# Optimization experiments

Hardware: AMD Instinct MI355X
Metric: run time of the kernel (lower is better)

The kernel has to match this reference:

```python
import jax, jax.numpy as jnp
import numpy as np

BATCH, INPUTDIM, OUTDIM, GRIDSIZE = 4096, 256, 256, 64


def setup_inputs() -> dict:
    key = jax.random.key(0)
    k1, k2 = jax.random.split(key)
    x = jax.random.normal(k1, (BATCH, INPUTDIM), dtype=jnp.float32)
    # xavier_uniform over (2, outdim, inputdim, gridsize): fan_in = inputdim*gridsize, fan_out = outdim*gridsize
    fan_in = INPUTDIM * GRIDSIZE
    fan_out = OUTDIM * GRIDSIZE
    limit = float(np.sqrt(6.0 / (fan_in + fan_out)))
    fouriercoeffs = jax.random.uniform(
        k2, (2, OUTDIM, INPUTDIM, GRIDSIZE), dtype=jnp.float32,
        minval=-limit, maxval=limit)
    bias = jnp.zeros((1, OUTDIM), dtype=jnp.float32)
    return {"x": x, "fouriercoeffs": fouriercoeffs, "bias": bias}


def reference(x, fouriercoeffs, bias):
    # x: [B, inputdim]; fouriercoeffs: [2, outdim, inputdim, gridsize]; bias: [1, outdim]
    # gridsize_param is clamp/round'ed to an int in torch -> static = initial_gridsize here.
    G = fouriercoeffs.shape[-1]
    k = jnp.arange(1, G + 1, dtype=x.dtype)        # [G] frequencies 1..G
    xk = x[:, :, None] * k                          # [B, inputdim, G]
    c = jnp.cos(xk)                                 # [B, inputdim, G]
    s = jnp.sin(xk)                                 # [B, inputdim, G]
    # Fused contraction over (inputdim, gridsize) -- avoids the naive
    # [B, outdim, inputdim, gridsize] broadcast tensor of the torch code.
    y = (jnp.einsum('big,oig->bo', c, fouriercoeffs[0])
         + jnp.einsum('big,oig->bo', s, fouriercoeffs[1])
         + bias)                                    # [B, outdim]
    return y
```

## Files before the change

### kernel.cpp

```cpp
#include <hip/hip_runtime.h>
#include <hip/hip_bf16.h>


typedef __attribute__((ext_vector_type(8))) short short8;
typedef __attribute__((ext_vector_type(16))) float f32x16;

#define SPLITK 16
#define ICHUNK (256 / SPLITK)

#define INV2PI 0.15915494309189535f

__device__ __forceinline__ unsigned short f2bf(float f) {
    unsigned u = __builtin_bit_cast(unsigned, f);
    u += 0x7fffu + ((u >> 16) & 1u);
    return (unsigned short)(u >> 16);
}
#if __has_builtin(__builtin_amdgcn_cvt_pk_bf16_f32)
typedef __attribute__((ext_vector_type(2))) __bf16 bf16x2_t;
__device__ __forceinline__ unsigned pkbf16(float a, float b) {
    bf16x2_t v = __builtin_amdgcn_cvt_pk_bf16_f32(a, b);
    return __builtin_bit_cast(unsigned, v);
}
#else
__device__ __forceinline__ unsigned pkbf16(float a, float b) {
    unsigned ua = __builtin_bit_cast(unsigned, a) + 0x8000u;
    unsigned ub = __builtin_bit_cast(unsigned, b) + 0x8000u;
    return __builtin_amdgcn_perm(ub, ua, 0x07060302u);
}
#endif

__device__ __forceinline__ void dbl2(float c, float s, float& co, float& so) {
    float t = c + c;
    co = __builtin_fmaf(t, c, -1.f);
    so = t * s;
}
__device__ __forceinline__ void rot2(float c, float s, float cr, float sr,
                                     float& co, float& so) {
    float t = s * sr;
    co = __builtin_fmaf(c, cr, -t);
    float u = s * cr;
    so = __builtin_fmaf(c, sr, u);
}

__device__ __forceinline__ short8 chain8(float m1, float fm1, float f0) {
    unsigned r[4];
    float vp = fm1, v = f0;
    #pragma unroll
    for (int h = 0; h < 4; ++h) {
        float v1 = __builtin_fmaf(m1, v, -vp);
        r[h] = pkbf16(v, v1);
        float v2 = __builtin_fmaf(m1, v1, -v);
        vp = v1; v = v2;
    }
    uint4 u; u.x = r[0]; u.y = r[1]; u.z = r[2]; u.w = r[3];
    return __builtin_bit_cast(short8, u);
}

__device__ __forceinline__ void async_load16(const void* g, void* l) {
    __builtin_amdgcn_global_load_lds(
        (const __attribute__((address_space(1))) unsigned int*)g,
        (__attribute__((address_space(3))) unsigned int*)l,
        16, 0, 0);
}

__global__ __launch_bounds__(512) void prep_kernel(
    const float* __restrict__ fc, unsigned short* __restrict__ ws2)
{
    __shared__ unsigned pk[512][36];
    const int i = blockIdx.x;
    const int t = threadIdx.x;
    const int rr  = t >> 4;
    const int l16 = t & 15;

    #pragma unroll
    for (int p = 0; p < 16; ++p) {
        int r = p * 32 + rr;
        const float4* src =
            (const float4*)(fc + ((size_t)r * 256 + i) * 64) + l16;
        float4 v = *src;
        pk[r][l16 * 2]     = pkbf16(v.x, v.y);
        pk[r][l16 * 2 + 1] = pkbf16(v.z, v.w);
    }
    __syncthreads();

    #pragma unroll
    for (int gg = 0; gg < 8; ++gg) {
        int gi = gg * 512 + t;
        int sog = gi >> 6, ll = gi & 63;
        int ks = sog >> 3, cb = sog & 7;
        int o  = cb * 32 + (ll & 31);
        int kb = ks * 16 + (ll >> 5) * 8;
        int tt = kb >> 6, g0 = kb & 63;
        int r = tt * 256 + o;
        int c = g0 >> 1;
        uint4 v;
        v.x = pk[r][c]; v.y = pk[r][c + 1];
        v.z = pk[r][c + 2]; v.w = pk[r][c + 3];
        ((uint4*)ws2)[(size_t)i * 4096 + gi] = v;
    }
}

__global__ __launch_bounds__(256) void bias_init(
    const float* __restrict__ bias, float* __restrict__ out)
{
    int idx4 = blockIdx.x * 256 + threadIdx.x;
    ((float4*)out)[idx4] = ((const float4*)bias)[idx4 & 63];
}

__global__ __launch_bounds__(256) void reduce_kernel(
    const unsigned short* __restrict__ pws, const float* __restrict__ bias,
    float* __restrict__ out)
{
    int idx4 = blockIdx.x * 256 + threadIdx.x;
    float4 r = ((const float4*)bias)[idx4 & 63];
    #pragma unroll
    for (int z = 0; z < SPLITK; ++z) {
        ushort4 v = ((const ushort4*)pws)[(size_t)z * 262144 + idx4];
        r.x += __builtin_bit_cast(float, (unsigned)v.x << 16);
        r.y += __builtin_bit_cast(float, (unsigned)v.y << 16);
        r.z += __builtin_bit_cast(float, (unsigned)v.z << 16);
        r.w += __builtin_bit_cast(float, (unsigned)v.w << 16);
    }
    ((float4*)out)[idx4] = r;
}

template <bool USE_WS, bool PARTIAL>
__global__ __launch_bounds__(512, 2) void fkan_gemm(
    const float* __restrict__ x, const float* __restrict__ fc,
    const unsigned short* __restrict__ bws, float* __restrict__ out,
    unsigned short* __restrict__ pws)
{
    __shared__ uint4 Bflat[8192];
    __shared__ float xs[ICHUNK][256];

    const int t  = threadIdx.x;
    const int l  = t & 63;
    const int w  = t >> 6;
    const int m32 = l & 31;
    const int h  = l >> 5;

    const int bid = blockIdx.x;
    const int z   = bid & 15;
    const int bx  = bid >> 4;
    const int rowBase = bx * 256;
    const int iBase   = z * ICHUNK;

    f32x16 acc[8];
    #pragma unroll
    for (int a = 0; a < 8; ++a) acc[a] = (f32x16)0.0f;

    short8 aF[8];

    auto stageHalf = [&](int slot, int j) {
        const uint4* base = (const uint4*)bws +
            (size_t)(iBase + (j >> 1)) * 4096 + (j & 1) * 2048;
        uint4* dst = Bflat + slot * 2048;
        #pragma unroll
        for (int cc = 0; cc < 4; ++cc) {
            int c = cc * 8 + w;
            async_load16(base + (size_t)c * 64 + l, (void*)(dst + c * 64));
        }
    };

    auto synth = [&](int ii) {
        float xv = xs[ii][w * 32 + m32];
        float rev = xv * INV2PI;
        float s1 = __builtin_amdgcn_sinf(rev);
        float c1 = __builtin_amdgcn_cosf(rev);
        const float m1 = c1 + c1;
        float c2, s2, c4, s4, c8, s8, c16, s16;
        dbl2(c1, s1, c2, s2);
        dbl2(c2, s2, c4, s4);
        dbl2(c4, s4, c8, s8);
        dbl2(c8, s8, c16, s16);
        float cB = h ? c8 : 1.f;
        float sB = h ? s8 : 0.f;
        #pragma unroll
        for (int k = 0; k < 4; ++k) {
            float cB1, sB1;
            rot2(cB, sB, c1, s1, cB1, sB1);
            aF[k]     = chain8(m1, cB, cB1);
            aF[4 + k] = chain8(m1, sB, sB1);
            if (k < 3) {
                float cN, sN;
                rot2(cB, sB, c16, s16, cN, sN);
                cB = cN; sB = sN;
            }
        }
    };

    auto mfmaHalf = [&](int slot, short8 a0, short8 a1, short8 a2, short8 a3) {
        const uint4* Bp = Bflat + slot * 2048;
        short8 av[4] = {a0, a1, a2, a3};
        #pragma unroll
        for (int ks = 0; ks < 4; ++ks) {
            short8 bF[8];
            #pragma unroll
            for (int cf = 0; cf < 8; ++cf)
                bF[cf] = __builtin_bit_cast(short8, Bp[(ks * 8 + cf) * 64 + l]);
            #pragma unroll
            for (int cf = 0; cf < 8; ++cf)
                acc[cf] = __builtin_amdgcn_mfma_f32_32x32x16_bf16(
                    av[ks], bF[cf], acc[cf], 0, 0, 0);
        }
    };

    auto loadXs = [&]() {
        const int row = t >> 1;
        const int hf  = t & 1;
        const float4* px =
            (const float4*)(x + (size_t)(rowBase + row) * 256 + iBase) + hf * 2;
        float4 v0 = px[0], v1 = px[1];
        int c0 = hf * 8;
        xs[c0 + 0][row] = v0.x; xs[c0 + 1][row] = v0.y;
        xs[c0 + 2][row] = v0.z; xs[c0 + 3][row] = v0.w;
        xs[c0 + 4][row] = v1.x; xs[c0 + 5][row] = v1.y;
        xs[c0 + 6][row] = v1.z; xs[c0 + 7][row] = v1.w;
    };

    if constexpr (USE_WS) {
        loadXs();
        stageHalf(0, 0);
        stageHalf(1, 1);
        stageHalf(2, 2);
        asm volatile("s_waitcnt vmcnt(8) lgkmcnt(0)" ::: "memory");
        __builtin_amdgcn_s_barrier();
        asm volatile("" ::: "memory");

        #pragma unroll 1
        for (int jj = 0; jj < 16; ++jj) {
            const int j0 = jj * 2;

            if (jj <= 14) stageHalf((j0 + 3) & 3, j0 + 3);
            synth(jj);
            __builtin_amdgcn_s_setprio(1);
            mfmaHalf(j0 & 3, aF[0], aF[1], aF[2], aF[3]);
            __builtin_amdgcn_s_setprio(0);
            if (jj < 15) asm volatile("s_waitcnt vmcnt(8)" ::: "memory");
            else         asm volatile("s_waitcnt vmcnt(0)" ::: "memory");
            __builtin_amdgcn_s_barrier();
            asm volatile("" ::: "memory");

            if (jj <= 13) stageHalf((j0 + 4) & 3, j0 + 4);
            __builtin_amdgcn_s_setprio(1);
            mfmaHalf((j0 + 1) & 3, aF[4], aF[5], aF[6], aF[7]);
            __builtin_amdgcn_s_setprio(0);
            if (jj < 14) {
                asm volatile("s_waitcnt vmcnt(8)" ::: "memory");
                __builtin_amdgcn_s_barrier();
                asm volatile("" ::: "memory");
            } else if (jj == 14) {
                asm volatile("s_waitcnt vmcnt(4)" ::: "memory");
                __builtin_amdgcn_s_barrier();
                asm volatile("" ::: "memory");
            }
        }
    } else {
        auto stageBfc = [&](int p, int i) {
            #pragma unroll
            for (int gg = 0; gg < 8; ++gg) {
                int gi  = gg * 512 + t;
                int sog = gi >> 6, ll = gi & 63;
                int ks = sog >> 3, cb = sog & 7;
                int o  = cb * 32 + (ll & 31);
                int kb = ks * 16 + (ll >> 5) * 8;
                int tt = kb >> 6, g0 = kb & 63;
                const float4* p4 = (const float4*)(fc +
                    ((((size_t)tt * 256 + o) * 256 + i) * 64 + g0));
                float4 a = p4[0], b = p4[1];
                uint4 v;
                v.x = pkbf16(a.x, a.y); v.y = pkbf16(a.z, a.w);
                v.z = pkbf16(b.x, b.y); v.w = pkbf16(b.z, b.w);
                Bflat[p * 4096 + gi] = v;
            }
        };
        stageBfc(0, iBase);
        loadXs();
        __syncthreads();
        #pragma unroll 1
        for (int ii = 0; ii < ICHUNK; ++ii) {
            const int p = ii & 1;
            if (ii + 1 < ICHUNK) stageBfc(p ^ 1, iBase + ii + 1);
            synth(ii);
            mfmaHalf(p * 2,     aF[0], aF[1], aF[2], aF[3]);
            mfmaHalf(p * 2 + 1, aF[4], aF[5], aF[6], aF[7]);
            __syncthreads();
        }
    }

    const int r0 = rowBase + w * 32 + h * 4;
    if (PARTIAL) {
        unsigned short* dst = pws + (size_t)z * (4096u * 256u);
        #pragma unroll
        for (int cf = 0; cf < 8; ++cf)
            #pragma unroll
            for (int e = 0; e < 16; ++e) {
                int rl = (e & 3) + 8 * (e >> 2);
                dst[(size_t)(r0 + rl) * 256 + (cf * 32 + m32)] =
                    f2bf(acc[cf][e]);
            }
    } else {
        #pragma unroll
        for (int cf = 0; cf < 8; ++cf)
            #pragma unroll
            for (int e = 0; e < 16; ++e) {
                int rl = (e & 3) + 8 * (e >> 2);
                atomicAdd(out + (size_t)(r0 + rl) * 256 + (cf * 32 + m32),
                          acc[cf][e]);
            }
    }
}

extern "C" void kernel_launch(void* const* d_in, const int* in_sizes, int n_in,
                              void* d_out, int out_size, void* d_ws, size_t ws_size,
                              hipStream_t stream) {
    const float* x    = (const float*)d_in[0];
    const float* fc   = (const float*)d_in[1];
    const float* bias = (const float*)d_in[2];
    float* out = (float*)d_out;
    unsigned short* bws = (unsigned short*)d_ws;

    const size_t wsCoeff = (size_t)256 * 4096 * 16;
    const size_t wsFull  = wsCoeff + (size_t)SPLITK * 4096 * 256 * 2;
    unsigned short* pws = (unsigned short*)((char*)d_ws + wsCoeff);

    if (ws_size >= wsFull) {
        hipLaunchKernelGGL(prep_kernel, dim3(256), dim3(512), 0, stream, fc, bws);
        hipLaunchKernelGGL((fkan_gemm<true, true>), dim3(256), dim3(512), 0, stream,
                           x, fc, bws, out, pws);
        hipLaunchKernelGGL(reduce_kernel, dim3(1024), dim3(256), 0, stream,
                           pws, bias, out);
    } else if (ws_size >= wsCoeff) {
        hipLaunchKernelGGL(bias_init, dim3(1024), dim3(256), 0, stream, bias, out);
        hipLaunchKernelGGL(prep_kernel, dim3(256), dim3(512), 0, stream, fc, bws);
        hipLaunchKernelGGL((fkan_gemm<true, false>), dim3(256), dim3(512), 0, stream,
                           x, fc, bws, out, pws);
    } else {
        hipLaunchKernelGGL(bias_init, dim3(1024), dim3(256), 0, stream, bias, out);
        hipLaunchKernelGGL((fkan_gemm<false, false>), dim3(256), dim3(512), 0, stream,
                           x, fc, bws, out, pws);
    }
}
```

Before: 150.5 us.

## Retile warp output to 64x128 to halve per-warp LDS B-fragment reads

Each warp now computes a 64-row by 128-column output tile (two row fragments by four column fragments) instead of 32 rows by all 256 columns. Each B fragment read from shared memory now feeds two MFMAs, which halves LDS traffic per MFMA. The cost is that every warp synthesizes sin/cos for two rows, so the two column-group warps repeat the same synthesis work, and register pressure for A fragments goes up.

Measured after the change: 156.9 us. +4.3%, slower.

```diff
diff --git a/kernel.cpp b/kernel.cpp
--- a/kernel.cpp
+++ b/kernel.cpp
@@ -136,6 +136,8 @@
     const int t  = threadIdx.x;
     const int l  = t & 63;
     const int w  = t >> 6;
+    const int rg = w >> 1;
+    const int cg = w & 1;
     const int m32 = l & 31;
     const int h  = l >> 5;
 
@@ -145,11 +147,13 @@
     const int rowBase = bx * 256;
     const int iBase   = z * ICHUNK;
 
-    f32x16 acc[8];
-    #pragma unroll
-    for (int a = 0; a < 8; ++a) acc[a] = (f32x16)0.0f;
-
-    short8 aF[8];
+    f32x16 acc[2][4];
+    #pragma unroll
+    for (int a = 0; a < 2; ++a)
+        #pragma unroll
+        for (int b = 0; b < 4; ++b) acc[a][b] = (f32x16)0.0f;
+
+    short8 aF[2][8];
 
     auto stageHalf = [&](int slot, int j) {
         const uint4* base = (const uint4*)bws +
@@ -163,45 +167,55 @@
     };
 
     auto synth = [&](int ii) {
-        float xv = xs[ii][w * 32 + m32];
-        float rev = xv * INV2PI;
-        float s1 = __builtin_amdgcn_sinf(rev);
-        float c1 = __builtin_amdgcn_cosf(rev);
-        const float m1 = c1 + c1;
-        float c2, s2, c4, s4, c8, s8, c16, s16;
-        dbl2(c1, s1, c2, s2);
-        dbl2(c2, s2, c4, s4);
-        dbl2(c4, s4, c8, s8);
-        dbl2(c8, s8, c16, s16);
-        float cB = h ? c8 : 1.f;
-        float sB = h ? s8 : 0.f;
-        #pragma unroll
-        for (int k = 0; k < 4; ++k) {
-            float cB1, sB1;
-            rot2(cB, sB, c1, s1, cB1, sB1);
-            aF[k]     = chain8(m1, cB, cB1);
-            aF[4 + k] = chain8(m1, sB, sB1);
-            if (k < 3) {
-                float cN, sN;
-                rot2(cB, sB, c16, s16, cN, sN);
-                cB = cN; sB = sN;
+        #pragma unroll
+        for (int rf = 0; rf < 2; ++rf) {
+            float xv = xs[ii][rg * 64 + rf * 32 + m32];
+            float rev = xv * INV2PI;
+            float s1 = __builtin_amdgcn_sinf(rev);
+            float c1 = __builtin_amdgcn_cosf(rev);
+            const float m1 = c1 + c1;
+            float c2, s2, c4, s4, c8, s8, c16, s16;
+            dbl2(c1, s1, c2, s2);
+            dbl2(c2, s2, c4, s4);
+            dbl2(c4, s4, c8, s8);
+            dbl2(c8, s8, c16, s16);
+            float cB = h ? c8 : 1.f;
+            float sB = h ? s8 : 0.f;
+            #pragma unroll
+            for (int k = 0; k < 4; ++k) {
+                float cB1, sB1;
+                rot2(cB, sB, c1, s1, cB1, sB1);
+                aF[rf][k]     = chain8(m1, cB, cB1);
+                aF[rf][4 + k] = chain8(m1, sB, sB1);
+                if (k < 3) {
+                    float cN, sN;
+                    rot2(cB, sB, c16, s16, cN, sN);
+                    cB = cN; sB = sN;
+                }
             }
         }
     };
 
-    auto mfmaHalf = [&](int slot, short8 a0, short8 a1, short8 a2, short8 a3) {
+    auto mfmaHalf = [&](int slot,
+                        short8 a00, short8 a01, short8 a02, short8 a03,
+                        short8 a10, short8 a11, short8 a12, short8 a13) {
         const uint4* Bp = Bflat + slot * 2048;
-        short8 av[4] = {a0, a1, a2, a3};
+        short8 a0v[4] = {a00, a01, a02, a03};
+        short8 a1v[4] = {a10, a11, a12, a13};
         #pragma unroll
         for (int ks = 0; ks < 4; ++ks) {
-            short8 bF[8];
-            #pragma unroll
-            for (int cf = 0; cf < 8; ++cf)
-                bF[cf] = __builtin_bit_cast(short8, Bp[(ks * 8 + cf) * 64 + l]);
-            #pragma unroll
-            for (int cf = 0; cf < 8; ++cf)
-                acc[cf] = __builtin_amdgcn_mfma_f32_32x32x16_bf16(
-                    av[ks], bF[cf], acc[cf], 0, 0, 0);
+            short8 bF[4];
+            #pragma unroll
+            for (int cf = 0; cf < 4; ++cf)
+                bF[cf] = __builtin_bit_cast(short8,
+                    Bp[(ks * 8 + cg * 4 + cf) * 64 + l]);
+            #pragma unroll
+            for (int cf = 0; cf < 4; ++cf) {
+                acc[0][cf] = __builtin_amdgcn_mfma_f32_32x32x16_bf16(
+                    a0v[ks], bF[cf], acc[0][cf], 0, 0, 0);
+                acc[1][cf] = __builtin_amdgcn_mfma_f32_32x32x16_bf16(
+                    a1v[ks], bF[cf], acc[1][cf], 0, 0, 0);
+            }
         }
     };
 
@@ -234,7 +248,9 @@
             if (jj <= 14) stageHalf((j0 + 3) & 3, j0 + 3);
             synth(jj);
             __builtin_amdgcn_s_setprio(1);
-            mfmaHalf(j0 & 3, aF[0], aF[1], aF[2], aF[3]);
+            mfmaHalf(j0 & 3,
+                     aF[0][0], aF[0][1], aF[0][2], aF[0][3],
+                     aF[1][0], aF[1][1], aF[1][2], aF[1][3]);
             __builtin_amdgcn_s_setprio(0);
             if (jj < 15) asm volatile("s_waitcnt vmcnt(8)" ::: "memory");
             else         asm volatile("s_waitcnt vmcnt(0)" ::: "memory");
@@ -243,7 +259,9 @@
 
             if (jj <= 13) stageHalf((j0 + 4) & 3, j0 + 4);
             __builtin_amdgcn_s_setprio(1);
-            mfmaHalf((j0 + 1) & 3, aF[4], aF[5], aF[6], aF[7]);
+            mfmaHalf((j0 + 1) & 3,
+                     aF[0][4], aF[0][5], aF[0][6], aF[0][7],
+                     aF[1][4], aF[1][5], aF[1][6], aF[1][7]);
             __builtin_amdgcn_s_setprio(0);
             if (jj < 14) {
                 asm volatile("s_waitcnt vmcnt(8)" ::: "memory");
@@ -282,32 +300,41 @@
             const int p = ii & 1;
             if (ii + 1 < ICHUNK) stageBfc(p ^ 1, iBase + ii + 1);
             synth(ii);
-            mfmaHalf(p * 2,     aF[0], aF[1], aF[2], aF[3]);
-            mfmaHalf(p * 2 + 1, aF[4], aF[5], aF[6], aF[7]);
+            mfmaHalf(p * 2,
+                     aF[0][0], aF[0][1], aF[0][2], aF[0][3],
+                     aF[1][0], aF[1][1], aF[1][2], aF[1][3]);
+            mfmaHalf(p * 2 + 1,
+                     aF[0][4], aF[0][5], aF[0][6], aF[0][7],
+                     aF[1][4], aF[1][5], aF[1][6], aF[1][7]);
             __syncthreads();
         }
     }
 
-    const int r0 = rowBase + w * 32 + h * 4;
+    const int r0 = rowBase + rg * 64 + h * 4;
+    const int c0 = cg * 128 + m32;
     if (PARTIAL) {
         unsigned short* dst = pws + (size_t)z * (4096u * 256u);
         #pragma unroll
-        for (int cf = 0; cf < 8; ++cf)
-            #pragma unroll
-            for (int e = 0; e < 16; ++e) {
-                int rl = (e & 3) + 8 * (e >> 2);
-                dst[(size_t)(r0 + rl) * 256 + (cf * 32 + m32)] =
-                    f2bf(acc[cf][e]);
-            }
+        for (int rf = 0; rf < 2; ++rf)
+            #pragma unroll
+            for (int cf = 0; cf < 4; ++cf)
+                #pragma unroll
+                for (int e = 0; e < 16; ++e) {
+                    int rl = (e & 3) + 8 * (e >> 2);
+                    dst[(size_t)(r0 + rf * 32 + rl) * 256 + (c0 + cf * 32)] =
+                        f2bf(acc[rf][cf][e]);
+                }
     } else {
         #pragma unroll
-        for (int cf = 0; cf < 8; ++cf)
-            #pragma unroll
-            for (int e = 0; e < 16; ++e) {
-                int rl = (e & 3) + 8 * (e >> 2);
-                atomicAdd(out + (size_t)(r0 + rl) * 256 + (cf * 32 + m32),
-                          acc[cf][e]);
-            }
+        for (int rf = 0; rf < 2; ++rf)
+            #pragma unroll
+            for (int cf = 0; cf < 4; ++cf)
+                #pragma unroll
+                for (int e = 0; e < 16; ++e) {
+                    int rl = (e & 3) + 8 * (e >> 2);
+                    atomicAdd(out + (size_t)(r0 + rf * 32 + rl) * 256 + (c0 + cf * 32),
+                              acc[rf][cf][e]);
+                }
     }
 }
 
```
